# Kernel tuning notes

Measured on AMD Instinct MI355X. Metric: run time of the kernel, lower is better.

Reference implementation:

```python
import jax, jax.numpy as jnp
import numpy as np

VIEW_R = 32
SCALING = 16.0 / 8.0  # lora_alpha / r


def setup_inputs() -> dict:
    key = jax.random.key(0)
    ks = jax.random.split(key, 12)
    bs, S, d, r = 64, 256, 768, 8
    n = d // VIEW_R  # 24
    return {
        "x": jax.random.normal(ks[0], (bs, S, d), jnp.float32),
        "user_h": jax.random.normal(ks[1], (bs, d), jnp.float32),
        "item_h": jax.random.normal(ks[2], (bs, d), jnp.float32),
        "W": jax.random.normal(ks[3], (d, d), jnp.float32) * 0.02,   # base weight (out,in)
        "b": jax.random.normal(ks[4], (d,), jnp.float32) * 0.02,
        "A": jax.random.normal(ks[5], (r, d), jnp.float32) * 0.02,   # lora_A
        "B": jax.random.normal(ks[6], (d, r), jnp.float32) * 0.02,   # lora_B (zeros at init; randomized to exercise math)
        "Wu": jax.random.normal(ks[7], (d, d), jnp.float32) * 0.02,  # lora_U weight (out,in)
        "VU": jax.random.normal(ks[8], (n, VIEW_R), jnp.float32) * 0.02,
        "Wi": jax.random.normal(ks[9], (d, d), jnp.float32) * 0.02,  # lora_I weight
        "VI": jax.random.normal(ks[10], (n, VIEW_R), jnp.float32) * 0.02,
    }


def _kron_branch(x, h, Wlin, V):
    # original: weight[b, q*n_in + n, l*32 + m] = (h @ Wlin.T)[b, q, l] * V[n, m]
    #           result[b,s,:] = x[b,s,:] @ weight[b]
    # factorized form (same math, no (bs, d, d) intermediate):
    bs, S, d = x.shape
    n, m = V.shape
    q = VIEW_R
    l = d // VIEW_R
    wq = (h @ Wlin.T).reshape(bs, q, l)          # (b, q, l)
    x4 = x.reshape(bs, S, q, n)                  # d split as (q, n)
    t = jnp.einsum("bsqn,nm->bsqm", x4, V)
    out = jnp.einsum("bsqm,bql->bslm", t, wq)    # out index = l*32 + m
    return out.reshape(bs, S, d)


def reference(x, user_h, item_h, W, b, A, B, Wu, VU, Wi, VI):
    # F.linear + LoRA
    out = jnp.einsum("bsd,od->bso", x, W) + b
    out = out + jnp.einsum("bsd,rd,or->bso", x, A, B) * SCALING
    # user Kronecker low-rank per-sample weight branch
    out = out + _kron_branch(x, user_h, Wu, VU)
    # item branch
    out = out + _kron_branch(x, item_h, Wi, VI)
    return out
```

## Files before the change

kernel.cpp:

```cpp
#include <hip/hip_runtime.h>
#include <hip/hip_bf16.h>

typedef __bf16 bf16x8 __attribute__((ext_vector_type(8)));
typedef float f32x4 __attribute__((ext_vector_type(4)));
typedef unsigned short u16x8 __attribute__((ext_vector_type(8)));

__device__ __forceinline__ unsigned short f2bf(float f) {
    unsigned int u = __builtin_bit_cast(unsigned int, f);
    unsigned int r = (u + 0x7FFFu + ((u >> 16) & 1u)) >> 16;
    return (unsigned short)r;
}

__device__ __forceinline__ void load_lds_16(const void* g, void* lds) {
    __builtin_amdgcn_global_load_lds(
        (const __attribute__((address_space(1))) unsigned int*)g,
        (__attribute__((address_space(3))) unsigned int*)lds, 16, 0, 0);
}

__global__ __launch_bounds__(256) void prep_kernel(
    const float* __restrict__ x, unsigned short* __restrict__ xb,
    const float* __restrict__ W, const float* __restrict__ A,
    const float* __restrict__ B, unsigned short* __restrict__ weffB,
    const float* __restrict__ uh, const float* __restrict__ ih,
    const float* __restrict__ Wu, const float* __restrict__ Wi,
    float* __restrict__ wqu, float* __restrict__ wqi) {
    __shared__ float Wl[64 * 68];
    __shared__ float Hl[16 * 68];
    const int bx = blockIdx.x;
    const int t = threadIdx.x;
    if (bx < 96) {
        const int br = bx / 48, rem = bx % 48;
        const int ot = rem >> 2, bt = rem & 3;
        const int o0 = ot * 64, b0 = bt * 16;
        const float* h = (br ? ih : uh);
        const float* Wm = (br ? Wi : Wu);
        const int so = t >> 2, sq = (t & 3) * 16;
        const int hr = t >> 4, hc = (t & 15) * 4;
        const int b_l = t >> 4, o4 = (t & 15) * 4;
        float acc0 = 0.f, acc1 = 0.f, acc2 = 0.f, acc3 = 0.f;
        for (int kk = 0; kk < 768; kk += 64) {
            const float* wrow = Wm + (o0 + so) * 768 + kk + sq;
            float4 w0 = ((const float4*)wrow)[0];
            float4 w1 = ((const float4*)wrow)[1];
            float4 w2 = ((const float4*)wrow)[2];
            float4 w3 = ((const float4*)wrow)[3];
            float4 hv = *(const float4*)(h + (b0 + hr) * 768 + kk + hc);
            Wl[(sq + 0) * 68 + so] = w0.x;  Wl[(sq + 1) * 68 + so] = w0.y;
            Wl[(sq + 2) * 68 + so] = w0.z;  Wl[(sq + 3) * 68 + so] = w0.w;
            Wl[(sq + 4) * 68 + so] = w1.x;  Wl[(sq + 5) * 68 + so] = w1.y;
            Wl[(sq + 6) * 68 + so] = w1.z;  Wl[(sq + 7) * 68 + so] = w1.w;
            Wl[(sq + 8) * 68 + so] = w2.x;  Wl[(sq + 9) * 68 + so] = w2.y;
            Wl[(sq + 10) * 68 + so] = w2.z; Wl[(sq + 11) * 68 + so] = w2.w;
            Wl[(sq + 12) * 68 + so] = w3.x; Wl[(sq + 13) * 68 + so] = w3.y;
            Wl[(sq + 14) * 68 + so] = w3.z; Wl[(sq + 15) * 68 + so] = w3.w;
            *(float4*)&Hl[hr * 68 + hc] = hv;
            __syncthreads();
#pragma unroll 8
            for (int k = 0; k < 64; ++k) {
                float hs = Hl[b_l * 68 + k];
                float4 wv = *(const float4*)&Wl[k * 68 + o4];
                acc0 += hs * wv.x; acc1 += hs * wv.y;
                acc2 += hs * wv.z; acc3 += hs * wv.w;
            }
            __syncthreads();
        }
        float* wq = (br ? wqi : wqu);
        float4 r; r.x = acc0; r.y = acc1; r.z = acc2; r.w = acc3;
        *(float4*)&wq[(b0 + b_l) * 768 + o0 + o4] = r;
    } else if (bx < 2400) {
        int idx = bx - 96;
        int o = idx / 3;
        int k = (idx % 3) * 256 + t;
        float acc = W[o * 768 + k];
#pragma unroll
        for (int r = 0; r < 8; ++r) acc += 2.0f * B[o * 8 + r] * A[r * 768 + k];
        weffB[o * 768 + k] = f2bf(acc);
    } else {
        int b2 = bx - 2400;
        const float4* xp = (const float4*)x;
        float4 a[4], c[4];
        int i0 = b2 * 1024 + t;
#pragma unroll
        for (int u = 0; u < 4; ++u) {
            int i = i0 + u * 256;
            a[u] = xp[i * 2];
            c[u] = xp[i * 2 + 1];
        }
#pragma unroll
        for (int u = 0; u < 4; ++u) {
            int i = i0 + u * 256;
            u16x8 r;
            r[0] = f2bf(a[u].x); r[1] = f2bf(a[u].y); r[2] = f2bf(a[u].z); r[3] = f2bf(a[u].w);
            r[4] = f2bf(c[u].x); r[5] = f2bf(c[u].y); r[6] = f2bf(c[u].z); r[7] = f2bf(c[u].w);
            *(u16x8*)(xb + (size_t)i * 8) = r;
        }
    }
}

__global__ __launch_bounds__(256, 3) void gemm_fused_kernel(
    const unsigned short* __restrict__ Xb, const unsigned short* __restrict__ WeffB,
    const float* __restrict__ VU, const float* __restrict__ VI,
    const float* __restrict__ wqu, const float* __restrict__ wqi,
    const float* __restrict__ bias, float* __restrict__ out) {
    __shared__ __align__(16) unsigned short As[128 * 64];
    __shared__ __align__(16) unsigned short Bs[128 * 64];
    __shared__ __align__(16) unsigned int vui[32 * 26];
    __shared__ __align__(16) float wqs[32 * 8];
    __shared__ float bias_s[128];
    const int tid = threadIdx.x;
    const int wave = tid >> 6, lane = tid & 63;
    const int id = blockIdx.x;
    const int nt = id >> 7, rem = id & 127, b = rem >> 1, mt = rem & 1;
    const int s0 = mt * 128, n0 = nt * 128;

    for (int i = tid; i < 768; i += 256) {
        int n = i >> 5, m = i & 31;
        vui[m * 26 + n] = ((unsigned int)f2bf(VU[i]) << 16) | (unsigned int)f2bf(VI[i]);
    }
    {
        int q = tid >> 3, g = (tid >> 1) & 3, br = tid & 1;
        const float* wq = br ? wqi : wqu;
        wqs[tid] = wq[b * 768 + q * 24 + nt * 4 + g];
    }
    if (tid < 128) bias_s[tid] = bias[n0 + tid];
    __syncthreads();

    const unsigned short* Abase = Xb + (size_t)(b * 256 + s0) * 768;
    const unsigned short* Bbase = WeffB + (size_t)n0 * 768;
    const int wm = wave & 1, wn = wave >> 1;
    const int lrow = lane >> 3, lcp = lane & 7;
    const int rg = tid >> 3, cc = tid & 7;
    const int sl = cc ^ (rg & 7);
    const unsigned short* Wp0 = Bbase + (size_t)rg * 768 + cc * 8;

    f32x4 acc[4][4] = {};
    u16x8 wreg[4];
#pragma unroll
    for (int g = 0; g < 4; ++g) wreg[g] = *(const u16x8*)(Wp0 + (size_t)g * 32 * 768);

    for (int kk = 0; kk < 768; kk += 64) {
#pragma unroll
        for (int u = 0; u < 4; ++u) {
            int tA = wave * 4 + u;
            int r = tA * 8 + lrow;
            int c = lcp ^ (r & 7);
            load_lds_16(Abase + (size_t)r * 768 + kk + c * 8, (void*)(As + tA * 512));
        }
        {
            int kb = kk + cc * 8;
            int q = (kb * 2731) >> 16;
            int n0c = kb - q * 24;
            const unsigned int* vp = &vui[rg * 26 + n0c];
            uint2 pv01 = *(const uint2*)(vp);
            uint2 pv23 = *(const uint2*)(vp + 2);
            uint2 pv45 = *(const uint2*)(vp + 4);
            uint2 pv67 = *(const uint2*)(vp + 6);
            unsigned int pv[8] = {pv01.x, pv01.y, pv23.x, pv23.y, pv45.x, pv45.y, pv67.x, pv67.y};
            float fu[8], fi[8];
#pragma unroll
            for (int j = 0; j < 8; ++j) {
                fu[j] = __builtin_bit_cast(float, pv[j] & 0xFFFF0000u);
                fi[j] = __builtin_bit_cast(float, pv[j] << 16);
            }
            const float4* wp4 = (const float4*)&wqs[q * 8];
            float4 wa = wp4[0], wb = wp4[1];
            float wu[4] = {wa.x, wa.z, wb.x, wb.z};
            float wi[4] = {wa.y, wa.w, wb.y, wb.w};
#pragma unroll
            for (int g = 0; g < 4; ++g) {
                u16x8 kv;
#pragma unroll
                for (int j = 0; j < 8; ++j) {
                    float wf = __builtin_bit_cast(float, (unsigned int)wreg[g][j] << 16);
                    float v = wf + fu[j] * wu[g];
                    v = v + fi[j] * wi[g];
                    kv[j] = (unsigned short)(__builtin_bit_cast(unsigned int, v) >> 16);
                }
                *(u16x8*)(Bs + (g * 32 + rg) * 64 + sl * 8) = kv;
            }
        }
        if (kk < 704) {
            const unsigned short* Wn = Wp0 + kk + 64;
#pragma unroll
            for (int g = 0; g < 4; ++g) wreg[g] = *(const u16x8*)(Wn + (size_t)g * 32 * 768);
        }
        __syncthreads();
#pragma unroll
        for (int h = 0; h < 2; ++h) {
            const int cb = h * 4 + (lane >> 4);
            const int rl = lane & 15;
            bf16x8 af[4], bw[4];
#pragma unroll
            for (int i = 0; i < 4; ++i) {
                int r = wm * 64 + i * 16 + rl;
                int c = cb ^ (r & 7);
                af[i] = *(const bf16x8*)(As + r * 64 + c * 8);
            }
#pragma unroll
            for (int j = 0; j < 4; ++j) {
                int r = wn * 64 + j * 16 + rl;
                int c = cb ^ (r & 7);
                bw[j] = *(const bf16x8*)(Bs + r * 64 + c * 8);
            }
#pragma unroll
            for (int i = 0; i < 4; ++i)
#pragma unroll
                for (int j = 0; j < 4; ++j)
                    acc[i][j] = __builtin_amdgcn_mfma_f32_16x16x32_bf16(af[i], bw[j], acc[i][j], 0, 0, 0);
        }
        __syncthreads();
    }

    const int cl = lane & 15, rq = lane >> 4;
#pragma unroll
    for (int j = 0; j < 4; ++j) {
        int nn = wn * 64 + j * 16 + cl;
        float bv = bias_s[nn];
#pragma unroll
        for (int i = 0; i < 4; ++i) {
            int mrow = s0 + wm * 64 + i * 16 + rq * 4;
            float* op = out + (size_t)(b * 256 + mrow) * 768 + n0 + nn;
#pragma unroll
            for (int g = 0; g < 4; ++g) op[(size_t)g * 768] = acc[i][j][g] + bv;
        }
    }
}

__global__ void weff_kernel(const float* __restrict__ W, const float* __restrict__ A,
                            const float* __restrict__ B, float* __restrict__ Weff) {
    int o = blockIdx.x / 3;
    int k = (blockIdx.x % 3) * 256 + threadIdx.x;
    float acc = W[o * 768 + k];
#pragma unroll
    for (int r = 0; r < 8; ++r) acc += 2.0f * B[o * 8 + r] * A[r * 768 + k];
    Weff[o * 768 + k] = acc;
}

__global__ void wq2_kernel(const float* __restrict__ uh, const float* __restrict__ ih,
                           const float* __restrict__ Wu, const float* __restrict__ Wi,
                           float* __restrict__ wqu, float* __restrict__ wqi) {
    int bx = blockIdx.x;
    int og = bx % 192;
    int rest = bx / 192;
    int b = rest & 63;
    int br = rest >> 6;
    int wave = threadIdx.x >> 6, lane = threadIdx.x & 63;
    int o = og * 4 + wave;
    const float* h = (br ? ih : uh) + b * 768;
    const float* Wrow = (br ? Wi : Wu) + (size_t)o * 768;
    const float4* hp = (const float4*)(h + lane * 12);
    const float4* wp = (const float4*)(Wrow + lane * 12);
    float s = 0.0f;
#pragma unroll
    for (int j = 0; j < 3; ++j) {
        float4 hv = hp[j], wv = wp[j];
        s += hv.x * wv.x + hv.y * wv.y + hv.z * wv.z + hv.w * wv.w;
    }
#pragma unroll
    for (int off = 32; off; off >>= 1) s += __shfl_down(s, off);
    if (lane == 0) (br ? wqi : wqu)[b * 768 + o] = s;
}

__global__ void naive_kernel(const float* __restrict__ x, const float* __restrict__ Weff,
                             const float* __restrict__ wqu, const float* __restrict__ wqi,
                             const float* __restrict__ VU, const float* __restrict__ VI,
                             const float* __restrict__ bias, float* __restrict__ out) {
    int bs_ = blockIdx.x / 3;
    int chunk = blockIdx.x % 3;
    int b = bs_ >> 8;
    __shared__ float xs[768];
    for (int i = threadIdx.x; i < 768; i += 256) xs[i] = x[(size_t)bs_ * 768 + i];
    __syncthreads();
    int o = chunk * 256 + threadIdx.x;
    int m = o & 31, l = o >> 5;
    float acc = bias[o];
    for (int q = 0; q < 32; ++q) {
        float wu = wqu[b * 768 + q * 24 + l];
        float wi = wqi[b * 768 + q * 24 + l];
#pragma unroll
        for (int n = 0; n < 24; ++n) {
            int k = q * 24 + n;
            float w = Weff[o * 768 + k] + VU[n * 32 + m] * wu + VI[n * 32 + m] * wi;
            acc += xs[k] * w;
        }
    }
    out[(size_t)bs_ * 768 + o] = acc;
}

extern "C" void kernel_launch(void* const* d_in, const int* in_sizes, int n_in,
                              void* d_out, int out_size, void* d_ws, size_t ws_size,
                              hipStream_t stream) {
    const float* x  = (const float*)d_in[0];
    const float* uh = (const float*)d_in[1];
    const float* ih = (const float*)d_in[2];
    const float* W  = (const float*)d_in[3];
    const float* bv = (const float*)d_in[4];
    const float* A  = (const float*)d_in[5];
    const float* B  = (const float*)d_in[6];
    const float* Wu = (const float*)d_in[7];
    const float* VU = (const float*)d_in[8];
    const float* Wi = (const float*)d_in[9];
    const float* VI = (const float*)d_in[10];
    float* out = (float*)d_out;

    const size_t off_xb   = 0;
    const size_t off_weff = 25165824;
    const size_t off_wqu  = off_weff + 1179648;
    const size_t off_wqi  = off_wqu + 196608;
    const size_t need     = off_wqi + 196608;

    char* ws = (char*)d_ws;
    if (ws_size >= need) {
        unsigned short* xb    = (unsigned short*)(ws + off_xb);
        unsigned short* weffB = (unsigned short*)(ws + off_weff);
        float* wqu = (float*)(ws + off_wqu);
        float* wqi = (float*)(ws + off_wqi);
        prep_kernel<<<3936, 256, 0, stream>>>(x, xb, W, A, B, weffB, uh, ih, Wu, Wi, wqu, wqi);
        gemm_fused_kernel<<<768, 256, 0, stream>>>(xb, weffB, VU, VI, wqu, wqi, bv, out);
    } else {
        float* weff = (float*)ws;
        float* wqu  = weff + 589824;
        float* wqi  = wqu + 49152;
        weff_kernel<<<2304, 256, 0, stream>>>(W, A, B, weff);
        wq2_kernel<<<24576, 256, 0, stream>>>(uh, ih, Wu, Wi, wqu, wqi);
        naive_kernel<<<49152, 256, 0, stream>>>(x, weff, wqu, wqi, VU, VI, bv, out);
    }
}
```

Baseline: 160.0 us.

## Split wq projection over K into partial sums reduced in GEMM prologue

The h @ Wlin.T projection in the prep kernel now runs as 384 blocks instead of 96. Each block handles a 96-wide K slice and a 32-row batch tile, and writes partial results to workspace. The fused GEMM sums the 8 partials when it loads wqs. This is meant to remove a long-running tail of a few blocks with serial K loops, at the cost of more workspace traffic and extra reads in the GEMM prologue. The B-tile modulation loop also switches to fmaf and v_perm packing of bf16 pairs, which removes per-element shifts.

```diff
diff --git a/kernel.cpp b/kernel.cpp
--- a/kernel.cpp
+++ b/kernel.cpp
@@ -23,52 +23,50 @@
     const float* __restrict__ B, unsigned short* __restrict__ weffB,
     const float* __restrict__ uh, const float* __restrict__ ih,
     const float* __restrict__ Wu, const float* __restrict__ Wi,
-    float* __restrict__ wqu, float* __restrict__ wqi) {
-    __shared__ float Wl[64 * 68];
-    __shared__ float Hl[16 * 68];
+    float* __restrict__ wqu_p, float* __restrict__ wqi_p) {
+    __shared__ __align__(16) float Wl[64 * 100];
+    __shared__ __align__(16) float Hl[32 * 100];
     const int bx = blockIdx.x;
     const int t = threadIdx.x;
-    if (bx < 96) {
-        const int br = bx / 48, rem = bx % 48;
-        const int ot = rem >> 2, bt = rem & 3;
-        const int o0 = ot * 64, b0 = bt * 16;
+    if (bx < 384) {
+        const int g = bx % 24, j = bx / 24;
+        const int br = g / 12, ot = g % 12;
+        const int bt = j & 1, ks = j >> 1;
+        const int o0 = ot * 64, b0 = bt * 32, k0 = ks * 96;
         const float* h = (br ? ih : uh);
         const float* Wm = (br ? Wi : Wu);
-        const int so = t >> 2, sq = (t & 3) * 16;
-        const int hr = t >> 4, hc = (t & 15) * 4;
-        const int b_l = t >> 4, o4 = (t & 15) * 4;
-        float acc0 = 0.f, acc1 = 0.f, acc2 = 0.f, acc3 = 0.f;
-        for (int kk = 0; kk < 768; kk += 64) {
-            const float* wrow = Wm + (o0 + so) * 768 + kk + sq;
-            float4 w0 = ((const float4*)wrow)[0];
-            float4 w1 = ((const float4*)wrow)[1];
-            float4 w2 = ((const float4*)wrow)[2];
-            float4 w3 = ((const float4*)wrow)[3];
-            float4 hv = *(const float4*)(h + (b0 + hr) * 768 + kk + hc);
-            Wl[(sq + 0) * 68 + so] = w0.x;  Wl[(sq + 1) * 68 + so] = w0.y;
-            Wl[(sq + 2) * 68 + so] = w0.z;  Wl[(sq + 3) * 68 + so] = w0.w;
-            Wl[(sq + 4) * 68 + so] = w1.x;  Wl[(sq + 5) * 68 + so] = w1.y;
-            Wl[(sq + 6) * 68 + so] = w1.z;  Wl[(sq + 7) * 68 + so] = w1.w;
-            Wl[(sq + 8) * 68 + so] = w2.x;  Wl[(sq + 9) * 68 + so] = w2.y;
-            Wl[(sq + 10) * 68 + so] = w2.z; Wl[(sq + 11) * 68 + so] = w2.w;
-            Wl[(sq + 12) * 68 + so] = w3.x; Wl[(sq + 13) * 68 + so] = w3.y;
-            Wl[(sq + 14) * 68 + so] = w3.z; Wl[(sq + 15) * 68 + so] = w3.w;
-            *(float4*)&Hl[hr * 68 + hc] = hv;
-            __syncthreads();
-#pragma unroll 8
-            for (int k = 0; k < 64; ++k) {
-                float hs = Hl[b_l * 68 + k];
-                float4 wv = *(const float4*)&Wl[k * 68 + o4];
-                acc0 += hs * wv.x; acc1 += hs * wv.y;
-                acc2 += hs * wv.z; acc3 += hs * wv.w;
-            }
-            __syncthreads();
-        }
-        float* wq = (br ? wqi : wqu);
-        float4 r; r.x = acc0; r.y = acc1; r.z = acc2; r.w = acc3;
-        *(float4*)&wq[(b0 + b_l) * 768 + o0 + o4] = r;
-    } else if (bx < 2400) {
-        int idx = bx - 96;
+        for (int i = t; i < 1536; i += 256) {
+            int row = i / 24, c = i % 24;
+            *(float4*)&Wl[row * 100 + c * 4] =
+                *(const float4*)(Wm + (size_t)(o0 + row) * 768 + k0 + c * 4);
+        }
+        for (int i = t; i < 768; i += 256) {
+            int row = i / 24, c = i % 24;
+            *(float4*)&Hl[row * 100 + c * 4] =
+                *(const float4*)(h + (size_t)(b0 + row) * 768 + k0 + c * 4);
+        }
+        __syncthreads();
+        const int o2 = t & 31, b4 = t >> 5;
+        float acc[2][4] = {};
+#pragma unroll 6
+        for (int k4 = 0; k4 < 24; ++k4) {
+            float4 w0 = *(const float4*)&Wl[o2 * 100 + k4 * 4];
+            float4 w1 = *(const float4*)&Wl[(o2 + 32) * 100 + k4 * 4];
+#pragma unroll
+            for (int jj = 0; jj < 4; ++jj) {
+                float4 hb = *(const float4*)&Hl[(b4 * 4 + jj) * 100 + k4 * 4];
+                acc[0][jj] += w0.x * hb.x + w0.y * hb.y + w0.z * hb.z + w0.w * hb.w;
+                acc[1][jj] += w1.x * hb.x + w1.y * hb.y + w1.z * hb.z + w1.w * hb.w;
+            }
+        }
+        float* part = (br ? wqi_p : wqu_p) + (size_t)ks * 49152;
+#pragma unroll
+        for (int oo = 0; oo < 2; ++oo)
+#pragma unroll
+            for (int jj = 0; jj < 4; ++jj)
+                part[(size_t)(b0 + b4 * 4 + jj) * 768 + o0 + o2 + oo * 32] = acc[oo][jj];
+    } else if (bx < 2688) {
+        int idx = bx - 384;
         int o = idx / 3;
         int k = (idx % 3) * 256 + t;
         float acc = W[o * 768 + k];
@@ -76,7 +74,7 @@
         for (int r = 0; r < 8; ++r) acc += 2.0f * B[o * 8 + r] * A[r * 768 + k];
         weffB[o * 768 + k] = f2bf(acc);
     } else {
-        int b2 = bx - 2400;
+        int b2 = bx - 2688;
         const float4* xp = (const float4*)x;
         float4 a[4], c[4];
         int i0 = b2 * 1024 + t;
@@ -100,7 +98,7 @@
 __global__ __launch_bounds__(256, 3) void gemm_fused_kernel(
     const unsigned short* __restrict__ Xb, const unsigned short* __restrict__ WeffB,
     const float* __restrict__ VU, const float* __restrict__ VI,
-    const float* __restrict__ wqu, const float* __restrict__ wqi,
+    const float* __restrict__ wqu_p, const float* __restrict__ wqi_p,
     const float* __restrict__ bias, float* __restrict__ out) {
     __shared__ __align__(16) unsigned short As[128 * 64];
     __shared__ __align__(16) unsigned short Bs[128 * 64];
@@ -118,9 +116,12 @@
         vui[m * 26 + n] = ((unsigned int)f2bf(VU[i]) << 16) | (unsigned int)f2bf(VI[i]);
     }
     {
-        int q = tid >> 3, g = (tid >> 1) & 3, br = tid & 1;
-        const float* wq = br ? wqi : wqu;
-        wqs[tid] = wq[b * 768 + q * 24 + nt * 4 + g];
+        int q = tid >> 3, g = (tid >> 1) & 3, brs = tid & 1;
+        const float* p = (brs ? wqi_p : wqu_p) + b * 768 + q * 24 + nt * 4 + g;
+        float s = 0.0f;
+#pragma unroll
+        for (int ks = 0; ks < 8; ++ks) s += p[(size_t)ks * 49152];
+        wqs[tid] = s;
     }
     if (tid < 128) bias_s[tid] = bias[n0 + tid];
     __syncthreads();
@@ -168,15 +169,21 @@
             float wi[4] = {wa.y, wa.w, wb.y, wb.w};
 #pragma unroll
             for (int g = 0; g < 4; ++g) {
-                u16x8 kv;
-#pragma unroll
-                for (int j = 0; j < 8; ++j) {
-                    float wf = __builtin_bit_cast(float, (unsigned int)wreg[g][j] << 16);
-                    float v = wf + fu[j] * wu[g];
-                    v = v + fi[j] * wi[g];
-                    kv[j] = (unsigned short)(__builtin_bit_cast(unsigned int, v) >> 16);
+                uint4 wd = __builtin_bit_cast(uint4, wreg[g]);
+                unsigned int warr[4] = {wd.x, wd.y, wd.z, wd.w};
+                unsigned int kvw[4];
+#pragma unroll
+                for (int p = 0; p < 4; ++p) {
+                    float lo = __builtin_bit_cast(float, warr[p] << 16);
+                    float hi = __builtin_bit_cast(float, warr[p] & 0xFFFF0000u);
+                    float v0 = fmaf(fi[2 * p],     wi[g], fmaf(fu[2 * p],     wu[g], lo));
+                    float v1 = fmaf(fi[2 * p + 1], wi[g], fmaf(fu[2 * p + 1], wu[g], hi));
+                    kvw[p] = __builtin_amdgcn_perm(__builtin_bit_cast(unsigned int, v1),
+                                                   __builtin_bit_cast(unsigned int, v0),
+                                                   0x07060302u);
                 }
-                *(u16x8*)(Bs + (g * 32 + rg) * 64 + sl * 8) = kv;
+                *(uint4*)(Bs + (g * 32 + rg) * 64 + sl * 8) =
+                    make_uint4(kvw[0], kvw[1], kvw[2], kvw[3]);
             }
         }
         if (kk < 704) {
@@ -306,17 +313,17 @@
     const size_t off_xb   = 0;
     const size_t off_weff = 25165824;
     const size_t off_wqu  = off_weff + 1179648;
-    const size_t off_wqi  = off_wqu + 196608;
-    const size_t need     = off_wqi + 196608;
+    const size_t off_wqi  = off_wqu + 1572864;
+    const size_t need     = off_wqi + 1572864;
 
     char* ws = (char*)d_ws;
     if (ws_size >= need) {
         unsigned short* xb    = (unsigned short*)(ws + off_xb);
         unsigned short* weffB = (unsigned short*)(ws + off_weff);
-        float* wqu = (float*)(ws + off_wqu);
-        float* wqi = (float*)(ws + off_wqi);
-        prep_kernel<<<3936, 256, 0, stream>>>(x, xb, W, A, B, weffB, uh, ih, Wu, Wi, wqu, wqi);
-        gemm_fused_kernel<<<768, 256, 0, stream>>>(xb, weffB, VU, VI, wqu, wqi, bv, out);
+        float* wqu_p = (float*)(ws + off_wqu);
+        float* wqi_p = (float*)(ws + off_wqi);
+        prep_kernel<<<4224, 256, 0, stream>>>(x, xb, W, A, B, weffB, uh, ih, Wu, Wi, wqu_p, wqi_p);
+        gemm_fused_kernel<<<768, 256, 0, stream>>>(xb, weffB, VU, VI, wqu_p, wqi_p, bv, out);
     } else {
         float* weff = (float*)ws;
         float* wqu  = weff + 589824;
```

Result: faster. 150.3 us (-6.1%).
